# Kernel tuning notes

Hardware: AMD Instinct MI355X
Metric: run time of the kernel (lower is better)

## Reference

```python
import jax, jax.numpy as jnp
import numpy as np

IN_DIM = 64
OUT_DIM = 64
NUM_HEADS = 4
NEG_SLOPE = 0.2
GAMMA = 1.0  # constraint_gamma
NUM_VARS = 100000
NUM_CLAUSES = 100000
NUM_CLUSTERS = 2048
VARS_PER = 64
CLAUSES_PER = 64
NUM_EDGES = 400000


def _xavier(k, shape):
    bound = np.sqrt(6.0 / (shape[0] + shape[1])).astype(np.float32)
    return jax.random.uniform(k, shape, jnp.float32, -bound, bound)


def setup_inputs() -> dict:
    key = jax.random.key(0)
    ks = jax.random.split(key, 11)
    return {
        "x_var": jax.random.normal(ks[0], (NUM_VARS, IN_DIM), jnp.float32),
        "x_clause": jax.random.normal(ks[1], (NUM_CLAUSES, IN_DIM), jnp.float32),
        "var_clause_edge_index": jax.random.randint(ks[2], (2, NUM_EDGES), 0, NUM_VARS),
        "edge_polarity": jax.random.normal(ks[3], (NUM_EDGES, 1), jnp.float32),
        "cluster_var_ids": jax.random.randint(ks[4], (NUM_CLUSTERS, VARS_PER), 0, NUM_VARS),
        "cluster_clause_ids": jax.random.randint(ks[5], (NUM_CLUSTERS, CLAUSES_PER), 0, NUM_CLAUSES),
        "satisfaction_scores": jax.random.uniform(ks[6], (NUM_CLAUSES,), jnp.float32),
        "active_heads": 4,
        "W_Q": _xavier(ks[7], (OUT_DIM, IN_DIM)),
        "W_K": _xavier(ks[8], (OUT_DIM, IN_DIM)),
        "W_V": _xavier(ks[9], (OUT_DIM, IN_DIM)),
        "head_weights": jnp.ones((NUM_HEADS,), jnp.float32),
        "out_proj_w": _xavier(ks[10], (OUT_DIM, OUT_DIM)),
        "out_proj_b": jnp.zeros((OUT_DIM,), jnp.float32),
    }


def reference(x_var, x_clause, var_clause_edge_index, edge_polarity,
              cluster_var_ids, cluster_clause_ids, satisfaction_scores,
              active_heads, W_Q, W_K, W_V, head_weights, out_proj_w, out_proj_b):
    # NOTE: var_clause_edge_index / edge_polarity are accepted but unused,
    # matching the original forward body.
    num_vars = x_var.shape[0]
    x_all = jnp.concatenate([x_var, x_clause], axis=0)            # [N, D]
    Q = x_all @ W_Q.T
    K = x_all @ W_K.T
    V = x_all @ W_V.T

    # Block-diagonal cluster layout: [C, S] with S = VARS_PER + CLAUSES_PER
    nodes = jnp.concatenate([cluster_var_ids, cluster_clause_ids + num_vars], axis=1)
    Qc = Q[nodes]                                                 # [C, S, D]
    Kc = K[nodes]
    Vc = V[nodes]

    scale = jnp.asarray(np.sqrt(OUT_DIM), Qc.dtype)
    scores = jnp.einsum('csd,ctd->cst', Qc, Kc) / scale            # [C, S, S]
    # constraint-aware bias on clause columns (added before leaky_relu)
    bias = jnp.concatenate(
        [jnp.zeros(cluster_var_ids.shape, scores.dtype),
         GAMMA * satisfaction_scores[cluster_clause_ids]], axis=1)  # [C, S]
    scores = jax.nn.leaky_relu(scores + bias[:, None, :], NEG_SLOPE)
    attn = jax.nn.softmax(scores, axis=-1)

    head_w = jnp.mean(head_weights[:active_heads])
    h = jnp.einsum('cst,ctd->csd', attn, Vc) * head_w             # [C, S, D]

    flat = nodes.reshape(-1)
    out = jnp.zeros_like(x_all).at[flat].add(h.reshape(-1, OUT_DIM))
    count = jnp.zeros((x_all.shape[0],), x_all.dtype).at[flat].add(1.0)
    out = out / jnp.maximum(count, 1.0)[:, None]
    out = out @ out_proj_w.T + out_proj_b

    return (x_var + out[:num_vars], x_clause + out[num_vars:])
```

## Files before the change

### kernel.cpp

```cpp
#include <hip/hip_runtime.h>


#define NV 100000
#define NN 200000
#define NCLUST 2048
#define XS 72

typedef __attribute__((ext_vector_type(8))) short short8;
typedef __attribute__((ext_vector_type(16))) float floatx16;

__device__ __forceinline__ unsigned short f2bf(float f) {
    union { float f; unsigned u; } v; v.f = f;
    unsigned r = v.u + 0x7fffu + ((v.u >> 16) & 1u);
    return (unsigned short)(r >> 16);
}
__device__ __forceinline__ unsigned pack2bf(float lo, float hi) {
    union { float f; unsigned u; } a, b; a.f = lo; b.f = hi;
    unsigned ra = a.u + 0x7fffu + ((a.u >> 16) & 1u);
    unsigned rb = b.u + 0x7fffu + ((b.u >> 16) & 1u);
    return (ra >> 16) | (rb & 0xffff0000u);
}
__device__ __forceinline__ int crow(int r, int lane) {
    return (r & 3) + 8 * (r >> 2) + 4 * (lane >> 5);
}
__device__ __forceinline__ void bar_lds() {
    __builtin_amdgcn_sched_barrier(0);
    asm volatile("s_waitcnt lgkmcnt(0)" ::: "memory");
    __builtin_amdgcn_s_barrier();
    __builtin_amdgcn_sched_barrier(0);
}

__global__ __launch_bounds__(256) void prep_kernel(
    const float* __restrict__ WQ, const float* __restrict__ WK,
    const float* __restrict__ WV, const float* __restrict__ Wout,
    const float* __restrict__ head_weights, const int* __restrict__ active_heads_p,
    unsigned short* __restrict__ Mtr, unsigned short* __restrict__ Pbf)
{
    int o = blockIdx.x * blockDim.x + threadIdx.x;
    int ah = active_heads_p[0];
    float hw = 0.f;
    for (int i = 0; i < ah; ++i) hw += head_weights[i];
    hw /= (float)ah;
    if (o < 4096) {
        int d = o >> 6, a = o & 63;
        float acc = 0.f;
        for (int j = 0; j < 64; ++j) acc += WQ[j*64 + a] * WK[j*64 + d];
        Mtr[o] = f2bf(acc * 0.125f);
    } else if (o < 8192) {
        int o2 = o - 4096;
        int j = o2 >> 6, b = o2 & 63;
        float acc = 0.f;
        for (int d = 0; d < 64; ++d) acc += Wout[j*64 + d] * WV[d*64 + b];
        Pbf[o2] = f2bf(acc * hw);
    }
}

template<bool WN>
__device__ __forceinline__ void cluster_compute(
    unsigned short* X, unsigned short* E,
    const int* ids, const float* biascl,
    const unsigned short* __restrict__ Mtr,
    unsigned short* __restrict__ accum_bf,
    int lane, int w, int m, int hk, int r, int cb,
    short8 nx0, short8 nx1, short8 nx2, short8 nx3)
{
    {
        floatx16 z0 = {}, z1 = {};
        #pragma unroll
        for (int ks = 0; ks < 4; ++ks) {
            short8 mb0 = *(const short8*)(Mtr + m * 64 + ks * 16 + hk);
            short8 mb1 = *(const short8*)(Mtr + (32 + m) * 64 + ks * 16 + hk);
            short8 a = *(const short8*)&X[(w * 32 + m) * XS + ks * 16 + hk];
            z0 = __builtin_amdgcn_mfma_f32_32x32x16_bf16(a, mb0, z0, 0, 0, 0);
            z1 = __builtin_amdgcn_mfma_f32_32x32x16_bf16(a, mb1, z1, 0, 0, 0);
        }
        #pragma unroll
        for (int rr = 0; rr < 16; ++rr) {
            int row = w * 32 + crow(rr, lane);
            E[row * XS + m]      = f2bf(z0[rr]);
            E[row * XS + 32 + m] = f2bf(z1[rr]);
        }
    }

    floatx16 sc[4] = {{}, {}, {}, {}};
    #pragma unroll
    for (int ks = 0; ks < 4; ++ks) {
        short8 a = *(const short8*)&E[(w * 32 + m) * XS + ks * 16 + hk];
        #pragma unroll
        for (int nt = 0; nt < 4; ++nt) {
            short8 b = *(const short8*)&X[(nt * 32 + m) * XS + ks * 16 + hk];
            sc[nt] = __builtin_amdgcn_mfma_f32_32x32x16_bf16(a, b, sc[nt], 0, 0, 0);
        }
    }

    const float b2 = biascl[m], b3 = biascl[32 + m];
    #pragma unroll
    for (int rr = 0; rr < 16; ++rr) {
        float a0 = sc[0][rr], a1 = sc[1][rr], a2 = sc[2][rr] + b2, a3 = sc[3][rr] + b3;
        a0 = a0 > 0.f ? a0 : 0.2f * a0;
        a1 = a1 > 0.f ? a1 : 0.2f * a1;
        a2 = a2 > 0.f ? a2 : 0.2f * a2;
        a3 = a3 > 0.f ? a3 : 0.2f * a3;
        a0 = __expf(a0); a1 = __expf(a1); a2 = __expf(a2); a3 = __expf(a3);
        float s4 = (a0 + a1) + (a2 + a3);
        #pragma unroll
        for (int off = 1; off < 32; off <<= 1) s4 += __shfl_xor(s4, off, 64);
        float inv = __builtin_amdgcn_rcpf(s4);
        sc[0][rr] = a0 * inv; sc[1][rr] = a1 * inv;
        sc[2][rr] = a2 * inv; sc[3][rr] = a3 * inv;
    }

    #pragma unroll
    for (int rr = 0; rr < 16; ++rr) {
        int row = w * 32 + crow(rr, lane);
        E[row * XS + m]      = f2bf(sc[0][rr]);
        E[row * XS + 32 + m] = f2bf(sc[1][rr]);
    }

    floatx16 g0 = {}, g1 = {};
    #pragma unroll
    for (int ks = 0; ks < 4; ++ks) {
        short8 a = *(const short8*)&E[(w * 32 + m) * XS + ks * 16 + hk];
        short8 b0, b1;
        #pragma unroll
        for (int j = 0; j < 8; ++j) {
            int t = ks * 16 + hk + j;
            b0[j] = (short)X[t * XS + m];
            b1[j] = (short)X[t * XS + 32 + m];
        }
        g0 = __builtin_amdgcn_mfma_f32_32x32x16_bf16(a, b0, g0, 0, 0, 0);
        g1 = __builtin_amdgcn_mfma_f32_32x32x16_bf16(a, b1, g1, 0, 0, 0);
    }

    #pragma unroll
    for (int rr = 0; rr < 16; ++rr) {
        int row = w * 32 + crow(rr, lane);
        E[row * XS + m]      = f2bf(sc[2][rr]);
        E[row * XS + 32 + m] = f2bf(sc[3][rr]);
    }

    #pragma unroll
    for (int ks = 0; ks < 4; ++ks) {
        short8 a = *(const short8*)&E[(w * 32 + m) * XS + ks * 16 + hk];
        short8 b0, b1;
        #pragma unroll
        for (int j = 0; j < 8; ++j) {
            int t = 64 + ks * 16 + hk + j;
            b0[j] = (short)X[t * XS + m];
            b1[j] = (short)X[t * XS + 32 + m];
        }
        g0 = __builtin_amdgcn_mfma_f32_32x32x16_bf16(a, b0, g0, 0, 0, 0);
        g1 = __builtin_amdgcn_mfma_f32_32x32x16_bf16(a, b1, g1, 0, 0, 0);
    }

    if (WN) {
        *(short8*)&E[r * XS + cb +  0] = nx0;
        *(short8*)&E[r * XS + cb +  8] = nx1;
        *(short8*)&E[r * XS + cb + 16] = nx2;
        *(short8*)&E[r * XS + cb + 24] = nx3;
    }

    const bool ev = !(lane & 1);
    const int colbase = ev ? m : (31 + m);
    #pragma unroll
    for (int rr = 0; rr < 16; ++rr) {
        int row = w * 32 + crow(rr, lane);
        int nid = ids[row];
        float a0 = g0[rr], a1 = g1[rr];
        float t0 = __shfl_xor(a0, 1, 64);
        float t1 = __shfl_xor(a1, 1, 64);
        float lo = ev ? a0 : t1;
        float hi = ev ? t0 : a1;
        unsigned pk = (unsigned)f2bf(lo) | ((unsigned)f2bf(hi) << 16);
        unsigned long long addr =
            (unsigned long long)(accum_bf + (size_t)nid * 64 + colbase);
        asm volatile("global_atomic_pk_add_bf16 %0, %1, off"
                     :: "v"(addr), "v"(pk) : "memory");
    }
}

__global__ __launch_bounds__(256, 4) void attn_kernel(
    const float* __restrict__ x_var, const float* __restrict__ x_clause,
    const int* __restrict__ cvar, const int* __restrict__ ccl,
    const float* __restrict__ sat, const unsigned short* __restrict__ Mtr,
    unsigned short* __restrict__ accum_bf, float* __restrict__ countv)
{
    __shared__ unsigned short bufA[128 * XS];
    __shared__ unsigned short bufB[128 * XS];
    __shared__ int   ids0[128], ids1[128];
    __shared__ float bias0[64], bias1[64];

    const int tid = threadIdx.x, lane = tid & 63, w = tid >> 6;
    const int m = lane & 31, hk = (lane >> 5) * 8;
    const int c0 = blockIdx.x * 2;
    const int r = tid >> 1, half = tid & 1, cb = half * 32;

    int nid0, nid1;
    const float *src0, *src1;
    float sv0 = 0.f, sv1 = 0.f;
    if (r < 64) {
        nid0 = cvar[c0 * 64 + r];
        nid1 = cvar[c0 * 64 + 64 + r];
        src0 = x_var + (size_t)nid0 * 64;
        src1 = x_var + (size_t)nid1 * 64;
    } else {
        int cid0 = ccl[c0 * 64 + (r - 64)];
        int cid1 = ccl[c0 * 64 + r];
        nid0 = NV + cid0; nid1 = NV + cid1;
        src0 = x_clause + (size_t)cid0 * 64;
        src1 = x_clause + (size_t)cid1 * 64;
        if (half) { sv0 = sat[cid0]; sv1 = sat[cid1]; }
    }

    const float4* s40 = (const float4*)src0 + half * 8;
    const float4* s41 = (const float4*)src1 + half * 8;
    float4 v0[8], v1[8];
    #pragma unroll
    for (int i = 0; i < 8; ++i) v0[i] = s40[i];
    #pragma unroll
    for (int i = 0; i < 8; ++i) v1[i] = s41[i];

    if (!half) {
        ids0[r] = nid0; ids1[r] = nid1;
        atomicAdd(&countv[nid0], 1.0f);
        atomicAdd(&countv[nid1], 1.0f);
    }
    if (r >= 64 && half) { bias0[r - 64] = sv0; bias1[r - 64] = sv1; }

    {
        union { unsigned u[16]; short8 v[4]; } h0;
        #pragma unroll
        for (int i = 0; i < 8; ++i) {
            h0.u[2*i]   = pack2bf(v0[i].x, v0[i].y);
            h0.u[2*i+1] = pack2bf(v0[i].z, v0[i].w);
        }
        #pragma unroll
        for (int i = 0; i < 4; ++i) *(short8*)&bufA[r * XS + cb + i * 8] = h0.v[i];
    }
    union { unsigned u[16]; short8 v[4]; } h1;
    #pragma unroll
    for (int i = 0; i < 8; ++i) {
        h1.u[2*i]   = pack2bf(v1[i].x, v1[i].y);
        h1.u[2*i+1] = pack2bf(v1[i].z, v1[i].w);
    }

    bar_lds();

    cluster_compute<true>(bufA, bufB, ids0, bias0, Mtr, accum_bf,
                          lane, w, m, hk, r, cb,
                          h1.v[0], h1.v[1], h1.v[2], h1.v[3]);

    bar_lds();

    short8 zz = {};
    cluster_compute<false>(bufB, bufA, ids1, bias1, Mtr, accum_bf,
                           lane, w, m, hk, r, cb, zz, zz, zz, zz);
}

__global__ __launch_bounds__(256, 4) void finalize_kernel(
    const float* __restrict__ x_var, const float* __restrict__ x_clause,
    const unsigned short* __restrict__ accum_bf, const float* __restrict__ countv,
    const unsigned short* __restrict__ Pbf, const float* __restrict__ bout,
    float* __restrict__ out)
{
    __shared__ float cnts[256];
    const int tid = threadIdx.x, lane = tid & 63, w = tid >> 6;
    const int base = blockIdx.x * 256;
    {
        int n = base + tid;
        cnts[tid] = (n < NN) ? countv[n] : 1.f;
    }
    __syncthreads();

    const int m = lane & 31, hk = (lane >> 5) * 8;
    short8 pb[2][4];
    #pragma unroll
    for (int nt = 0; nt < 2; ++nt)
        #pragma unroll
        for (int ks = 0; ks < 4; ++ks)
            pb[nt][ks] = *(const short8*)(Pbf + (nt * 32 + m) * 64 + ks * 16 + hk);
    const float bias0 = bout[m], bias1 = bout[32 + m];

    #pragma unroll
    for (int tm = 0; tm < 2; ++tm) {
        int mt = w * 2 + tm;
        const unsigned short* arow = accum_bf + (size_t)(base + mt * 32 + m) * 64;
        floatx16 c0 = {}, c1 = {};
        #pragma unroll
        for (int ks = 0; ks < 4; ++ks) {
            short8 a = *(const short8*)(arow + ks * 16 + hk);
            c0 = __builtin_amdgcn_mfma_f32_32x32x16_bf16(a, pb[0][ks], c0, 0, 0, 0);
            c1 = __builtin_amdgcn_mfma_f32_32x32x16_bf16(a, pb[1][ks], c1, 0, 0, 0);
        }
        #pragma unroll
        for (int rr = 0; rr < 16; ++rr) {
            int lrow = mt * 32 + crow(rr, lane);
            int n = base + lrow;
            if (n < NN) {
                float inv = 1.0f / fmaxf(cnts[lrow], 1.0f);
                const float* xs = (n < NV) ? (x_var + (size_t)n * 64)
                                           : (x_clause + (size_t)(n - NV) * 64);
                out[(size_t)n * 64 + m]      = xs[m]      + c0[rr] * inv + bias0;
                out[(size_t)n * 64 + 32 + m] = xs[32 + m] + c1[rr] * inv + bias1;
            }
        }
    }
}

extern "C" void kernel_launch(void* const* d_in, const int* in_sizes, int n_in,
                              void* d_out, int out_size, void* d_ws, size_t ws_size,
                              hipStream_t stream)
{
    const float* x_var        = (const float*)d_in[0];
    const float* x_clause     = (const float*)d_in[1];
    const int*   cvar         = (const int*)d_in[4];
    const int*   ccl          = (const int*)d_in[5];
    const float* sat          = (const float*)d_in[6];
    const int*   active_heads = (const int*)d_in[7];
    const float* WQ           = (const float*)d_in[8];
    const float* WK           = (const float*)d_in[9];
    const float* WV           = (const float*)d_in[10];
    const float* head_weights = (const float*)d_in[11];
    const float* Wout         = (const float*)d_in[12];
    const float* bout         = (const float*)d_in[13];

    unsigned short* accum_bf = (unsigned short*)d_ws;
    float* countv = (float*)(accum_bf + (size_t)NN * 64);
    unsigned short* Mtr = (unsigned short*)(countv + NN);
    unsigned short* Pbf = Mtr + 4096;

    hipMemsetAsync(accum_bf, 0, (size_t)NN * 64 * 2 + (size_t)NN * 4, stream);
    prep_kernel<<<32, 256, 0, stream>>>(WQ, WK, WV, Wout, head_weights, active_heads, Mtr, Pbf);
    attn_kernel<<<NCLUST / 2, 256, 0, stream>>>(x_var, x_clause, cvar, ccl, sat, Mtr, accum_bf, countv);
    finalize_kernel<<<(NN + 255) / 256, 256, 0, stream>>>(x_var, x_clause, accum_bf, countv, Pbf, bout, (float*)d_out);
}
```

Measured before the change: 214.5 us.

## Fuse workspace zeroing into prep kernel and coalesce finalize stores via LDS

Replaces the separate hipMemsetAsync with a grid-stride zeroing loop inside prep_kernel, now launched with 1024 blocks, which removes one launch and overlaps the clearing with the weight-product precompute. The finalize kernel now stages each MFMA output tile, already scaled and biased, into shared memory. Threads then read the residual input and write the output as contiguous float4 rows instead of scattered scalar stores. The cost is extra LDS use and bank traffic in finalize, and the weight-product work in prep now shares its blocks with the zeroing.

```diff
diff --git a/kernel.cpp b/kernel.cpp
--- a/kernel.cpp
+++ b/kernel.cpp
@@ -8,6 +8,7 @@
 
 typedef __attribute__((ext_vector_type(8))) short short8;
 typedef __attribute__((ext_vector_type(16))) float floatx16;
+typedef __attribute__((ext_vector_type(4))) unsigned uint4v;
 
 __device__ __forceinline__ unsigned short f2bf(float f) {
     union { float f; unsigned u; } v; v.f = f;
@@ -30,29 +31,33 @@
     __builtin_amdgcn_sched_barrier(0);
 }
 
+#define ZU4 1650000
 __global__ __launch_bounds__(256) void prep_kernel(
     const float* __restrict__ WQ, const float* __restrict__ WK,
     const float* __restrict__ WV, const float* __restrict__ Wout,
     const float* __restrict__ head_weights, const int* __restrict__ active_heads_p,
-    unsigned short* __restrict__ Mtr, unsigned short* __restrict__ Pbf)
+    unsigned short* __restrict__ Mtr, unsigned short* __restrict__ Pbf,
+    uint4v* __restrict__ zbase)
 {
     int o = blockIdx.x * blockDim.x + threadIdx.x;
-    int ah = active_heads_p[0];
-    float hw = 0.f;
-    for (int i = 0; i < ah; ++i) hw += head_weights[i];
-    hw /= (float)ah;
     if (o < 4096) {
         int d = o >> 6, a = o & 63;
         float acc = 0.f;
         for (int j = 0; j < 64; ++j) acc += WQ[j*64 + a] * WK[j*64 + d];
         Mtr[o] = f2bf(acc * 0.125f);
     } else if (o < 8192) {
+        int ah = active_heads_p[0];
+        float hw = 0.f;
+        for (int i = 0; i < ah; ++i) hw += head_weights[i];
+        hw /= (float)ah;
         int o2 = o - 4096;
         int j = o2 >> 6, b = o2 & 63;
         float acc = 0.f;
         for (int d = 0; d < 64; ++d) acc += Wout[j*64 + d] * WV[d*64 + b];
         Pbf[o2] = f2bf(acc * hw);
     }
+    uint4v z = {0u, 0u, 0u, 0u};
+    for (int j = o; j < ZU4; j += 262144) zbase[j] = z;
 }
 
 template<bool WN>
@@ -263,6 +268,7 @@
     const unsigned short* __restrict__ Pbf, const float* __restrict__ bout,
     float* __restrict__ out)
 {
+    __shared__ float T[4][32][68];
     __shared__ float cnts[256];
     const int tid = threadIdx.x, lane = tid & 63, w = tid >> 6;
     const int base = blockIdx.x * 256;
@@ -281,6 +287,8 @@
             pb[nt][ks] = *(const short8*)(Pbf + (nt * 32 + m) * 64 + ks * 16 + hk);
     const float bias0 = bout[m], bias1 = bout[32 + m];
 
+    const int r2 = lane >> 1, cb2 = (lane & 1) * 32;
+
     #pragma unroll
     for (int tm = 0; tm < 2; ++tm) {
         int mt = w * 2 + tm;
@@ -294,14 +302,24 @@
         }
         #pragma unroll
         for (int rr = 0; rr < 16; ++rr) {
-            int lrow = mt * 32 + crow(rr, lane);
-            int n = base + lrow;
-            if (n < NN) {
-                float inv = 1.0f / fmaxf(cnts[lrow], 1.0f);
-                const float* xs = (n < NV) ? (x_var + (size_t)n * 64)
-                                           : (x_clause + (size_t)(n - NV) * 64);
-                out[(size_t)n * 64 + m]      = xs[m]      + c0[rr] * inv + bias0;
-                out[(size_t)n * 64 + 32 + m] = xs[32 + m] + c1[rr] * inv + bias1;
+            int lr32 = crow(rr, lane);
+            float inv = 1.0f / fmaxf(cnts[mt * 32 + lr32], 1.0f);
+            T[w][lr32][m]      = c0[rr] * inv + bias0;
+            T[w][lr32][32 + m] = c1[rr] * inv + bias1;
+        }
+        int n2 = base + mt * 32 + r2;
+        if (n2 < NN) {
+            const float* xr = (n2 < NV) ? (x_var + (size_t)n2 * 64)
+                                        : (x_clause + (size_t)(n2 - NV) * 64);
+            float* orow = out + (size_t)n2 * 64;
+            #pragma unroll
+            for (int j = 0; j < 8; ++j) {
+                float4 t = *(const float4*)&T[w][r2][cb2 + 4 * j];
+                float4 xv = *(const float4*)&xr[cb2 + 4 * j];
+                float4 o;
+                o.x = t.x + xv.x; o.y = t.y + xv.y;
+                o.z = t.z + xv.z; o.w = t.w + xv.w;
+                *(float4*)&orow[cb2 + 4 * j] = o;
             }
         }
     }
@@ -329,8 +347,11 @@
     unsigned short* Mtr = (unsigned short*)(countv + NN);
     unsigned short* Pbf = Mtr + 4096;
 
-    hipMemsetAsync(accum_bf, 0, (size_t)NN * 64 * 2 + (size_t)NN * 4, stream);
-    prep_kernel<<<32, 256, 0, stream>>>(WQ, WK, WV, Wout, head_weights, active_heads, Mtr, Pbf);
-    attn_kernel<<<NCLUST / 2, 256, 0, stream>>>(x_var, x_clause, cvar, ccl, sat, Mtr, accum_bf, countv);
-    finalize_kernel<<<(NN + 255) / 256, 256, 0, stream>>>(x_var, x_clause, accum_bf, countv, Pbf, bout, (float*)d_out);
-}
+    prep_kernel<<<1024, 256, 0, stream>>>(WQ, WK, WV, Wout, head_weights,
+                                          active_heads, Mtr, Pbf,
+                                          (uint4v*)d_ws);
+    attn_kernel<<<NCLUST / 2, 256, 0, stream>>>(
+        x_var, x_clause, cvar, ccl, sat, Mtr, accum_bf, countv);
+    finalize_kernel<<<(NN + 255) / 256, 256, 0, stream>>>(
+        x_var, x_clause, accum_bf, countv, Pbf, bout, (float*)d_out);
+}
```

After: 209.7 us. 2.2% less time.

## Apply value/output projection per cluster before scatter, simplify finalize, fuse zeroing into prep

Applied to the files above, without the earlier changes.

Applies the combined V·Wout projection to each cluster's node features inside the attention kernel (X·P written back into LDS) before the attention-weighted sum. The accumulated rows then already hold projected outputs, so finalize becomes a plain vectorised elementwise pass with no MFMA. The workspace memset is replaced by a zeroing loop inside a larger prep launch. This adds per-cluster MFMA work and extra barriers in the attention kernel in exchange for a much lighter finalize and one fewer launch.

```diff
diff --git a/kernel.cpp b/kernel.cpp
--- a/kernel.cpp
+++ b/kernel.cpp
@@ -8,11 +8,15 @@
 
 typedef __attribute__((ext_vector_type(8))) short short8;
 typedef __attribute__((ext_vector_type(16))) float floatx16;
+typedef __attribute__((ext_vector_type(4))) unsigned uint4v;
 
 __device__ __forceinline__ unsigned short f2bf(float f) {
     union { float f; unsigned u; } v; v.f = f;
     unsigned r = v.u + 0x7fffu + ((v.u >> 16) & 1u);
     return (unsigned short)(r >> 16);
+}
+__device__ __forceinline__ float bf2f(unsigned short s) {
+    union { unsigned u; float f; } v; v.u = (unsigned)s << 16; return v.f;
 }
 __device__ __forceinline__ unsigned pack2bf(float lo, float hi) {
     union { float f; unsigned u; } a, b; a.f = lo; b.f = hi;
@@ -30,29 +34,33 @@
     __builtin_amdgcn_sched_barrier(0);
 }
 
+#define ZU4 1650000
 __global__ __launch_bounds__(256) void prep_kernel(
     const float* __restrict__ WQ, const float* __restrict__ WK,
     const float* __restrict__ WV, const float* __restrict__ Wout,
     const float* __restrict__ head_weights, const int* __restrict__ active_heads_p,
-    unsigned short* __restrict__ Mtr, unsigned short* __restrict__ Pbf)
+    unsigned short* __restrict__ Mtr, unsigned short* __restrict__ Pbf,
+    uint4v* __restrict__ zbase)
 {
     int o = blockIdx.x * blockDim.x + threadIdx.x;
-    int ah = active_heads_p[0];
-    float hw = 0.f;
-    for (int i = 0; i < ah; ++i) hw += head_weights[i];
-    hw /= (float)ah;
     if (o < 4096) {
         int d = o >> 6, a = o & 63;
         float acc = 0.f;
         for (int j = 0; j < 64; ++j) acc += WQ[j*64 + a] * WK[j*64 + d];
         Mtr[o] = f2bf(acc * 0.125f);
     } else if (o < 8192) {
+        int ah = active_heads_p[0];
+        float hw = 0.f;
+        for (int i = 0; i < ah; ++i) hw += head_weights[i];
+        hw /= (float)ah;
         int o2 = o - 4096;
         int j = o2 >> 6, b = o2 & 63;
         float acc = 0.f;
         for (int d = 0; d < 64; ++d) acc += Wout[j*64 + d] * WV[d*64 + b];
         Pbf[o2] = f2bf(acc * hw);
     }
+    uint4v z = {0u, 0u, 0u, 0u};
+    for (int j = o; j < ZU4; j += 262144) zbase[j] = z;
 }
 
 template<bool WN>
@@ -60,6 +68,7 @@
     unsigned short* X, unsigned short* E,
     const int* ids, const float* biascl,
     const unsigned short* __restrict__ Mtr,
+    const unsigned short* __restrict__ Pbf,
     unsigned short* __restrict__ accum_bf,
     int lane, int w, int m, int hk, int r, int cb,
     short8 nx0, short8 nx1, short8 nx2, short8 nx3)
@@ -90,6 +99,29 @@
         for (int nt = 0; nt < 4; ++nt) {
             short8 b = *(const short8*)&X[(nt * 32 + m) * XS + ks * 16 + hk];
             sc[nt] = __builtin_amdgcn_mfma_f32_32x32x16_bf16(a, b, sc[nt], 0, 0, 0);
+        }
+    }
+
+    bar_lds();
+
+    {
+        short8 xa[4];
+        #pragma unroll
+        for (int ks = 0; ks < 4; ++ks)
+            xa[ks] = *(const short8*)&X[(w * 32 + m) * XS + ks * 16 + hk];
+        floatx16 xp0 = {}, xp1 = {};
+        #pragma unroll
+        for (int ks = 0; ks < 4; ++ks) {
+            short8 p0 = *(const short8*)(Pbf + m * 64 + ks * 16 + hk);
+            short8 p1 = *(const short8*)(Pbf + (32 + m) * 64 + ks * 16 + hk);
+            xp0 = __builtin_amdgcn_mfma_f32_32x32x16_bf16(xa[ks], p0, xp0, 0, 0, 0);
+            xp1 = __builtin_amdgcn_mfma_f32_32x32x16_bf16(xa[ks], p1, xp1, 0, 0, 0);
+        }
+        #pragma unroll
+        for (int rr = 0; rr < 16; ++rr) {
+            int row = w * 32 + crow(rr, lane);
+            X[row * XS + m]      = f2bf(xp0[rr]);
+            X[row * XS + 32 + m] = f2bf(xp1[rr]);
         }
     }
 
@@ -109,6 +141,8 @@
         sc[0][rr] = a0 * inv; sc[1][rr] = a1 * inv;
         sc[2][rr] = a2 * inv; sc[3][rr] = a3 * inv;
     }
+
+    bar_lds();
 
     #pragma unroll
     for (int rr = 0; rr < 16; ++rr) {
@@ -183,6 +217,7 @@
     const float* __restrict__ x_var, const float* __restrict__ x_clause,
     const int* __restrict__ cvar, const int* __restrict__ ccl,
     const float* __restrict__ sat, const unsigned short* __restrict__ Mtr,
+    const unsigned short* __restrict__ Pbf,
     unsigned short* __restrict__ accum_bf, float* __restrict__ countv)
 {
     __shared__ unsigned short bufA[128 * XS];
@@ -246,64 +281,46 @@
 
     bar_lds();
 
-    cluster_compute<true>(bufA, bufB, ids0, bias0, Mtr, accum_bf,
+    cluster_compute<true>(bufA, bufB, ids0, bias0, Mtr, Pbf, accum_bf,
                           lane, w, m, hk, r, cb,
                           h1.v[0], h1.v[1], h1.v[2], h1.v[3]);
 
     bar_lds();
 
     short8 zz = {};
-    cluster_compute<false>(bufB, bufA, ids1, bias1, Mtr, accum_bf,
+    cluster_compute<false>(bufB, bufA, ids1, bias1, Mtr, Pbf, accum_bf,
                            lane, w, m, hk, r, cb, zz, zz, zz, zz);
 }
 
-__global__ __launch_bounds__(256, 4) void finalize_kernel(
+__global__ __launch_bounds__(256) void finalize_kernel(
     const float* __restrict__ x_var, const float* __restrict__ x_clause,
-    const unsigned short* __restrict__ accum_bf, const float* __restrict__ countv,
-    const unsigned short* __restrict__ Pbf, const float* __restrict__ bout,
-    float* __restrict__ out)
-{
-    __shared__ float cnts[256];
-    const int tid = threadIdx.x, lane = tid & 63, w = tid >> 6;
-    const int base = blockIdx.x * 256;
-    {
-        int n = base + tid;
-        cnts[tid] = (n < NN) ? countv[n] : 1.f;
-    }
-    __syncthreads();
-
-    const int m = lane & 31, hk = (lane >> 5) * 8;
-    short8 pb[2][4];
-    #pragma unroll
-    for (int nt = 0; nt < 2; ++nt)
-        #pragma unroll
-        for (int ks = 0; ks < 4; ++ks)
-            pb[nt][ks] = *(const short8*)(Pbf + (nt * 32 + m) * 64 + ks * 16 + hk);
-    const float bias0 = bout[m], bias1 = bout[32 + m];
-
-    #pragma unroll
-    for (int tm = 0; tm < 2; ++tm) {
-        int mt = w * 2 + tm;
-        const unsigned short* arow = accum_bf + (size_t)(base + mt * 32 + m) * 64;
-        floatx16 c0 = {}, c1 = {};
-        #pragma unroll
-        for (int ks = 0; ks < 4; ++ks) {
-            short8 a = *(const short8*)(arow + ks * 16 + hk);
-            c0 = __builtin_amdgcn_mfma_f32_32x32x16_bf16(a, pb[0][ks], c0, 0, 0, 0);
-            c1 = __builtin_amdgcn_mfma_f32_32x32x16_bf16(a, pb[1][ks], c1, 0, 0, 0);
-        }
-        #pragma unroll
-        for (int rr = 0; rr < 16; ++rr) {
-            int lrow = mt * 32 + crow(rr, lane);
-            int n = base + lrow;
-            if (n < NN) {
-                float inv = 1.0f / fmaxf(cnts[lrow], 1.0f);
-                const float* xs = (n < NV) ? (x_var + (size_t)n * 64)
-                                           : (x_clause + (size_t)(n - NV) * 64);
-                out[(size_t)n * 64 + m]      = xs[m]      + c0[rr] * inv + bias0;
-                out[(size_t)n * 64 + 32 + m] = xs[32 + m] + c1[rr] * inv + bias1;
-            }
-        }
+    const unsigned short* __restrict__ acc, const float* __restrict__ countv,
+    const float* __restrict__ bout, float* __restrict__ out)
+{
+    const int t0 = blockIdx.x * 256 + threadIdx.x;
+    const int o8 = t0 & 7;
+    const int co = o8 * 8;
+    const float4 b0 = *(const float4*)&bout[co];
+    const float4 b1 = *(const float4*)&bout[co + 4];
+    for (int i = t0; i < NN * 8; i += 2048 * 256) {
+        int n = i >> 3;
+        float inv = 1.0f / fmaxf(countv[n], 1.0f);
+        const float* xr = (n < NV) ? (x_var + (size_t)n * 64)
+                                   : (x_clause + (size_t)(n - NV) * 64);
+        short8 a = *(const short8*)(acc + (size_t)n * 64 + co);
+        float4 x0 = *(const float4*)(xr + co);
+        float4 x1 = *(const float4*)(xr + co + 4);
+        float4 o0, o1;
+        o0.x = x0.x + bf2f((unsigned short)a[0]) * inv + b0.x;
+        o0.y = x0.y + bf2f((unsigned short)a[1]) * inv + b0.y;
+        o0.z = x0.z + bf2f((unsigned short)a[2]) * inv + b0.z;
+        o0.w = x0.w + bf2f((unsigned short)a[3]) * inv + b0.w;
+        o1.x = x1.x + bf2f((unsigned short)a[4]) * inv + b1.x;
+        o1.y = x1.y + bf2f((unsigned short)a[5]) * inv + b1.y;
+        o1.z = x1.z + bf2f((unsigned short)a[6]) * inv + b1.z;
+        o1.w = x1.w + bf2f((unsigned short)a[7]) * inv + b1.w;
+        *(float4*)(out + (size_t)n * 64 + co)     = o0;
+        *(float4*)(out + (size_t)n * 64 + co + 4) = o1;
     }
 }
 
@@ -329,8 +346,11 @@
     unsigned short* Mtr = (unsigned short*)(countv + NN);
     unsigned short* Pbf = Mtr + 4096;
 
-    hipMemsetAsync(accum_bf, 0, (size_t)NN * 64 * 2 + (size_t)NN * 4, stream);
-    prep_kernel<<<32, 256, 0, stream>>>(WQ, WK, WV, Wout, head_weights, active_heads, Mtr, Pbf);
-    attn_kernel<<<NCLUST / 2, 256, 0, stream>>>(x_var, x_clause, cvar, ccl, sat, Mtr, accum_bf, countv);
-    finalize_kernel<<<(NN + 255) / 256, 256, 0, stream>>>(x_var, x_clause, accum_bf, countv, Pbf, bout, (float*)d_out);
-}
+    prep_kernel<<<1024, 256, 0, stream>>>(WQ, WK, WV, Wout, head_weights,
+                                          active_heads, Mtr, Pbf,
+                                          (uint4v*)d_ws);
+    attn_kernel<<<NCLUST / 2, 256, 0, stream>>>(
+        x_var, x_clause, cvar, ccl, sat, Mtr, Pbf, accum_bf, countv);
+    finalize_kernel<<<2048, 256, 0, stream>>>(
+        x_var, x_clause, accum_bf, countv, bout, (float*)d_out);
+}
```

Result: slower. 222.7 us (+3.8%).
